# Kernel tuning notes

Hardware: AMD Instinct MI355X
Metric: run time of the kernel (lower is better)

The kernel has to match this reference:

```python
import math
import jax, jax.numpy as jnp
import numpy as np

B, S, D, H, DK, DV = 4, 2048, 512, 8, 64, 64

def setup_inputs() -> dict:
    key = jax.random.key(0)
    ks = jax.random.split(key, 6)
    x = jax.random.normal(ks[0], (B, S, D), jnp.float32)
    W_Q = jax.random.normal(ks[1], (H, D, DK), jnp.float32) / D
    W_K = jax.random.normal(ks[2], (H, D, DK), jnp.float32) / D
    W_V = jax.random.normal(ks[3], (H, D, DV), jnp.float32) / D
    W_G = jax.random.normal(ks[4], (D, H * DV), jnp.float32) / D
    W_O = jax.random.normal(ks[5], (H * DV, D), jnp.float32) / D
    return {"x": x, "W_Q": W_Q, "W_K": W_K, "W_V": W_V, "W_G": W_G, "W_O": W_O}

def _decay_matrix(n_heads, seq_len, dtype):
    # gammas per head, exactly as in __init__
    gammas = 1.0 - jnp.exp(jnp.linspace(math.log(1.0 / 32), math.log(1.0 / 512), n_heads))
    n = jnp.arange(seq_len)
    diff = n[:, None] - n[None, :]                      # [S,S]
    mask = diff >= 0
    safe = jnp.where(mask, diff, 0)
    dec = jnp.where(mask[None], gammas[:, None, None].astype(dtype) ** safe[None], 0.0)
    return dec                                           # [H,S,S]

def reference(x, W_Q, W_K, W_V, W_G, W_O):
    Bx, Sx, Dx = x.shape
    Hn = W_Q.shape[0]
    dv = W_V.shape[-1]
    # per-head projections (all heads vectorized)
    Q = jnp.einsum('bsd,hdk->bhsk', x, W_Q)
    K = jnp.einsum('bsd,hdk->bhsk', x, W_K)
    V = jnp.einsum('bsd,hdv->bhsv', x, W_V)
    Dmat = _decay_matrix(Hn, Sx, x.dtype)                # [H,S,S] causal decay
    # retention scores: QK^T elementwise-weighted by decay (no softmax)
    A = jnp.einsum('bhsk,bhtk->bhst', Q, K) * Dmat[None]  # [B,H,S,S] == self_retentions
    ret = jnp.einsum('bhst,bhtv->bhsv', A, V)            # [B,H,S,dv]
    out_heads = ret.transpose(0, 2, 1, 3).reshape(Bx, Sx, Hn * dv)  # concat over heads
    # GroupNorm(num_groups=H, num_channels=H) applied to reshape(-1, H):
    # each group has exactly 1 element -> mean == x, var == 0 -> output is 0.
    eps = 1e-5
    flat = out_heads.reshape(-1, Hn)
    mean = flat
    var = jnp.zeros_like(flat)
    Y = ((flat - mean) * jax.lax.rsqrt(var + eps)).reshape(out_heads.shape)
    # swish-gated output projection
    g = x @ W_G
    out = (g * jax.nn.sigmoid(g) * Y) @ W_O              # [B,S,D]
    return out, A
```

## Files before the change

kernel.cpp:

```cpp
#include <hip/hip_runtime.h>
#include <hip/hip_bf16.h>
#include <math.h>

#define B_ 4
#define S_ 2048
#define D_ 512
#define H_ 8
#define DK_ 64

typedef __bf16 bf16x8 __attribute__((ext_vector_type(8)));
typedef float f32x16 __attribute__((ext_vector_type(16)));
typedef float f32x4 __attribute__((ext_vector_type(4)));

static __device__ __forceinline__ unsigned short f2bf(float f) {
    unsigned int u = __builtin_bit_cast(unsigned int, f);
    unsigned int r = (u + 0x7FFFu + ((u >> 16) & 1u)) >> 16;
    return (unsigned short)r;
}

__global__ __launch_bounds__(256) void k_setup(const float* __restrict__ wq, const float* __restrict__ wk,
                                               unsigned short* __restrict__ wqT, unsigned short* __restrict__ wkT,
                                               float* __restrict__ tab, float* __restrict__ out0) {
    const int bx = blockIdx.x;
    if (bx < 2048) {
        int idx = bx * 256 + threadIdx.x;
        const int n = H_ * DK_ * D_;
        const float* src = idx < n ? wq : wk;
        unsigned short* dst = idx < n ? wqT : wkT;
        int o = idx < n ? idx : idx - n;
        int d  = o % D_;
        int hk = o / D_;
        int k  = hk % DK_;
        int h  = hk / DK_;
        dst[o] = f2bf(src[(h * D_ + d) * DK_ + k]);
    } else if (bx < 2112) {
        int i = (bx - 2048) * 256 + threadIdx.x;
        if (i < H_ * S_) {
            int h = i / S_;
            int n = i % S_;
            double xv = -3.4657359027997265 - (double)h * (2.772588722239781 / 7.0);
            double g = 1.0 - exp(xv);
            tab[i] = (float)pow(g, (double)n);
        }
    } else {
        f32x4* base = reinterpret_cast<f32x4*>(out0) + (size_t)(bx - 2112) * 32768;
        f32x4 z = {0.f, 0.f, 0.f, 0.f};
#pragma unroll
        for (int j = 0; j < 128; ++j)
            base[threadIdx.x + j * 256] = z;
    }
}

__global__ __launch_bounds__(256) void k_fill_upper(float* __restrict__ aout) {
    const int bh = blockIdx.y;
    f32x4 z = {0.f, 0.f, 0.f, 0.f};
    int r = blockIdx.x;
    int g = 0, cum = 0;
    for (; g < 7; ++g) { int cnt = 4 * (7 - g); if (r < cum + cnt) break; cum += cnt; }
    const int rr  = r - cum;
    const int per = 7 - g;
    const int panel = g * 4 + rr / per;
    const int st    = g + 1 + rr % per;

    float* base = aout + (size_t)bh * S_ * S_ + (size_t)(panel * 64) * S_ + st * 256;
    const int t = threadIdx.x;
#pragma unroll
    for (int j = 0; j < 16; ++j) {
        int u = t + j * 256;
        int row = u >> 6;
        int c4  = u & 63;
        *reinterpret_cast<f32x4*>(base + (size_t)row * S_ + c4 * 4) = z;
    }
}

__global__ __launch_bounds__(256, 2) void k_proj(const float* __restrict__ x,
                                                 const unsigned short* __restrict__ wqT,
                                                 const unsigned short* __restrict__ wkT,
                                                 unsigned short* __restrict__ qb,
                                                 unsigned short* __restrict__ kb) {
    const int tid  = threadIdx.x;
    const int lane = tid & 63;
    const int wave = tid >> 6;
    const int m0   = blockIdx.x * 32;
    const int half = blockIdx.y;
    const unsigned short* wt = half ? wkT : wqT;
    unsigned short* outp     = half ? kb  : qb;

    __shared__ unsigned short atile[32 * 520];

    {
        const float4* xsrc = reinterpret_cast<const float4*>(x + (size_t)m0 * D_);
#pragma unroll
        for (int i = 0; i < 16; ++i) {
            int u   = tid + i * 256;
            int row = u >> 7, c4 = u & 127;
            float4 v = xsrc[u];
            ushort4 o;
            o.x = f2bf(v.x); o.y = f2bf(v.y); o.z = f2bf(v.z); o.w = f2bf(v.w);
            *reinterpret_cast<ushort4*>(&atile[row * 520 + c4 * 4]) = o;
        }
    }
    __syncthreads();

    const int row  = lane & 31;
    const int col  = lane & 31;
    const int hi   = lane >> 5;
    const int koff = hi * 8;
    const int n0   = wave * 128;

    const unsigned short* b0 = wt + (size_t)(n0 +  0 + row) * D_ + koff;
    const unsigned short* b1 = wt + (size_t)(n0 + 32 + row) * D_ + koff;
    const unsigned short* b2 = wt + (size_t)(n0 + 64 + row) * D_ + koff;
    const unsigned short* b3 = wt + (size_t)(n0 + 96 + row) * D_ + koff;
    const unsigned short* ap = atile + row * 520 + koff;

    f32x16 acc0 = {}, acc1 = {}, acc2 = {}, acc3 = {};
#pragma unroll
    for (int kk = 0; kk < D_; kk += 16) {
        bf16x8 a = *reinterpret_cast<const bf16x8*>(ap + kk);
        acc0 = __builtin_amdgcn_mfma_f32_32x32x16_bf16(a, *reinterpret_cast<const bf16x8*>(b0 + kk), acc0, 0, 0, 0);
        acc1 = __builtin_amdgcn_mfma_f32_32x32x16_bf16(a, *reinterpret_cast<const bf16x8*>(b1 + kk), acc1, 0, 0, 0);
        acc2 = __builtin_amdgcn_mfma_f32_32x32x16_bf16(a, *reinterpret_cast<const bf16x8*>(b2 + kk), acc2, 0, 0, 0);
        acc3 = __builtin_amdgcn_mfma_f32_32x32x16_bf16(a, *reinterpret_cast<const bf16x8*>(b3 + kk), acc3, 0, 0, 0);
    }

#define EPI(ACC, NB) { \
    int n = n0 + (NB) * 32 + col; \
    int hh = n >> 6, k = n & 63; \
    _Pragma("unroll") \
    for (int r = 0; r < 16; ++r) { \
        int rowD = (r & 3) + 8 * (r >> 2) + 4 * hi; \
        int m = m0 + rowD; \
        int bidx = m >> 11, s = m & 2047; \
        outp[(((size_t)bidx * H_ + hh) * S_ + s) * DK_ + k] = f2bf(ACC[r]); \
    } }
    EPI(acc0, 0) EPI(acc1, 1) EPI(acc2, 2) EPI(acc3, 3)
#undef EPI
}

__global__ __launch_bounds__(256) void k_score(const unsigned short* __restrict__ qb,
                                               const unsigned short* __restrict__ kb,
                                               const float* __restrict__ tab,
                                               float* __restrict__ aout) {
    const int lane = threadIdx.x & 63;
    const int w    = threadIdx.x >> 6;
    const int id   = blockIdx.x;
    const int c    = id & 7, sidx = id >> 3;
    const int bh   = (c >> 1) + 4 * (sidx >> 3);
    const int p    = ((sidx & 7) << 1) | (c & 1);
    const int h    = bh & (H_ - 1);
    float* ablk = aout + (size_t)bh * S_ * S_;
    const float* th = tab + h * S_;

    __shared__ float tile[64 * 256];

    const int col  = lane & 31;
    const int hi   = lane >> 5;
    const int koff = hi * 8;

    const float c1 = 1.0f / th[col];
    float grc[16];
    int rowDv[16];
#pragma unroll
    for (int r = 0; r < 16; ++r) {
        rowDv[r] = (r & 3) + 8 * (r >> 2) + 4 * hi;
        grc[r] = th[rowDv[r]] * c1;
    }

    for (int pp = 0; pp < 2; ++pp) {
        const int panel = pp ? (31 - p) : p;
        const int s0 = panel * 64;
        const int qq = panel >> 2;
        const int rb = panel & 3;

        bf16x8 qf[2][4];
#pragma unroll
        for (int rg = 0; rg < 2; ++rg) {
            const unsigned short* qp = qb + ((size_t)bh * S_ + s0 + rg * 32 + col) * DK_ + koff;
#pragma unroll
            for (int i = 0; i < 4; ++i)
                qf[rg][i] = *reinterpret_cast<const bf16x8*>(qp + 16 * i);
        }

        for (int st = 0; st <= qq; ++st) {
            const int t0 = st * 256;
            const int ct0 = t0 + w * 64;
            const bool active = (st < qq) || (w <= rb);
            if (active) {
                f32x16 acc[2][2] = {{{}, {}}, {{}, {}}};
#pragma unroll
                for (int cg = 0; cg < 2; ++cg) {
                    const unsigned short* kp = kb + ((size_t)bh * S_ + ct0 + cg * 32 + col) * DK_ + koff;
                    bf16x8 kf0 = *reinterpret_cast<const bf16x8*>(kp);
                    bf16x8 kf1 = *reinterpret_cast<const bf16x8*>(kp + 16);
                    bf16x8 kf2 = *reinterpret_cast<const bf16x8*>(kp + 32);
                    bf16x8 kf3 = *reinterpret_cast<const bf16x8*>(kp + 48);
#pragma unroll
                    for (int rg = 0; rg < 2; ++rg) {
                        acc[rg][cg] = __builtin_amdgcn_mfma_f32_32x32x16_bf16(qf[rg][0], kf0, acc[rg][cg], 0, 0, 0);
                        acc[rg][cg] = __builtin_amdgcn_mfma_f32_32x32x16_bf16(qf[rg][1], kf1, acc[rg][cg], 0, 0, 0);
                        acc[rg][cg] = __builtin_amdgcn_mfma_f32_32x32x16_bf16(qf[rg][2], kf2, acc[rg][cg], 0, 0, 0);
                        acc[rg][cg] = __builtin_amdgcn_mfma_f32_32x32x16_bf16(qf[rg][3], kf3, acc[rg][cg], 0, 0, 0);
                    }
                }
                if (st < qq || w < rb) {
#pragma unroll
                    for (int rg = 0; rg < 2; ++rg) {
#pragma unroll
                        for (int cg = 0; cg < 2; ++cg) {
                            const float sc = th[s0 + rg * 32 - ct0 - cg * 32];
#pragma unroll
                            for (int r = 0; r < 16; ++r)
                                tile[(rg * 32 + rowDv[r]) * 256 + w * 64 + cg * 32 + col] =
                                    acc[rg][cg][r] * grc[r] * sc;
                        }
                    }
                } else {
#pragma unroll
                    for (int rg = 0; rg < 2; ++rg) {
#pragma unroll
                        for (int cg = 0; cg < 2; ++cg) {
                            const int dbase = 32 * (rg - cg);
#pragma unroll
                            for (int r = 0; r < 16; ++r) {
                                int d = dbase + rowDv[r] - col;
                                float v = (d >= 0) ? acc[rg][cg][r] * th[d] : 0.0f;
                                tile[(rg * 32 + rowDv[r]) * 256 + w * 64 + cg * 32 + col] = v;
                            }
                        }
                    }
                }
            } else {
                f32x4 z = {0.f, 0.f, 0.f, 0.f};
#pragma unroll
                for (int i = 0; i < 16; ++i) {
                    int r = i * 4 + (lane >> 4);
                    int cc = (lane & 15) * 4;
                    *reinterpret_cast<f32x4*>(&tile[r * 256 + w * 64 + cc]) = z;
                }
            }
            __syncthreads();
#pragma unroll
            for (int r = 0; r < 16; ++r) {
                int row = w * 16 + r;
                f32x4 v = *reinterpret_cast<const f32x4*>(&tile[row * 256 + lane * 4]);
                *reinterpret_cast<f32x4*>(ablk + (size_t)(s0 + row) * S_ + t0 + lane * 4) = v;
            }
            __syncthreads();
        }
    }
}

extern "C" void kernel_launch(void* const* d_in, const int* in_sizes, int n_in,
                              void* d_out, int out_size, void* d_ws, size_t ws_size,
                              hipStream_t stream) {
    const float* x  = (const float*)d_in[0];
    const float* wq = (const float*)d_in[1];
    const float* wk = (const float*)d_in[2];

    char* ws = (char*)d_ws;
    unsigned short* wqT = (unsigned short*)(ws);
    unsigned short* wkT = (unsigned short*)(ws + 524288);
    unsigned short* qb  = (unsigned short*)(ws + 1048576);
    unsigned short* kb  = (unsigned short*)(ws + 9437184);
    float*          tab = (float*)(ws + 17825792);

    float* out0 = (float*)d_out;
    float* aout = (float*)d_out + (size_t)B_ * S_ * D_;

    hipLaunchKernelGGL(k_setup, dim3(2144), dim3(256), 0, stream,
                       wq, wk, wqT, wkT, tab, out0);
    hipLaunchKernelGGL(k_proj, dim3(B_*S_/32, 2), dim3(256), 0, stream,
                       x, wqT, wkT, qb, kb);
    hipLaunchKernelGGL(k_score, dim3(512), dim3(256), 0, stream,
                       qb, kb, tab, aout);
    hipLaunchKernelGGL(k_fill_upper, dim3(112, 32), dim3(256), 0, stream, aout);
}
```

Baseline: 178.3 us.

## Fuse upper-triangle zero fill and output zeroing into score kernel

Merges the separate upper-triangle zero-fill kernel and the out0 zeroing into the score kernel. Each of the 512 blocks zero-fills 7 upper tiles plus a slice of out0, with odd blocks filling before scoring and even blocks after, so zero stores overlap with compute in other blocks. This removes one kernel launch and the tail between kernels, but makes each score block do more store work.

After: 166.8 us. 1.07x faster.

```diff
diff --git a/kernel.cpp b/kernel.cpp
--- a/kernel.cpp
+++ b/kernel.cpp
@@ -20,7 +20,7 @@
 
 __global__ __launch_bounds__(256) void k_setup(const float* __restrict__ wq, const float* __restrict__ wk,
                                                unsigned short* __restrict__ wqT, unsigned short* __restrict__ wkT,
-                                               float* __restrict__ tab, float* __restrict__ out0) {
+                                               float* __restrict__ tab) {
     const int bx = blockIdx.x;
     if (bx < 2048) {
         int idx = bx * 256 + threadIdx.x;
@@ -33,7 +33,7 @@
         int k  = hk % DK_;
         int h  = hk / DK_;
         dst[o] = f2bf(src[(h * D_ + d) * DK_ + k]);
-    } else if (bx < 2112) {
+    } else {
         int i = (bx - 2048) * 256 + threadIdx.x;
         if (i < H_ * S_) {
             int h = i / S_;
@@ -42,34 +42,6 @@
             double g = 1.0 - exp(xv);
             tab[i] = (float)pow(g, (double)n);
         }
-    } else {
-        f32x4* base = reinterpret_cast<f32x4*>(out0) + (size_t)(bx - 2112) * 32768;
-        f32x4 z = {0.f, 0.f, 0.f, 0.f};
-#pragma unroll
-        for (int j = 0; j < 128; ++j)
-            base[threadIdx.x + j * 256] = z;
-    }
-}
-
-__global__ __launch_bounds__(256) void k_fill_upper(float* __restrict__ aout) {
-    const int bh = blockIdx.y;
-    f32x4 z = {0.f, 0.f, 0.f, 0.f};
-    int r = blockIdx.x;
-    int g = 0, cum = 0;
-    for (; g < 7; ++g) { int cnt = 4 * (7 - g); if (r < cum + cnt) break; cum += cnt; }
-    const int rr  = r - cum;
-    const int per = 7 - g;
-    const int panel = g * 4 + rr / per;
-    const int st    = g + 1 + rr % per;
-
-    float* base = aout + (size_t)bh * S_ * S_ + (size_t)(panel * 64) * S_ + st * 256;
-    const int t = threadIdx.x;
-#pragma unroll
-    for (int j = 0; j < 16; ++j) {
-        int u = t + j * 256;
-        int row = u >> 6;
-        int c4  = u & 63;
-        *reinterpret_cast<f32x4*>(base + (size_t)row * S_ + c4 * 4) = z;
     }
 }
 
@@ -138,21 +110,17 @@
 #undef EPI
 }
 
-__global__ __launch_bounds__(256) void k_score(const unsigned short* __restrict__ qb,
-                                               const unsigned short* __restrict__ kb,
-                                               const float* __restrict__ tab,
-                                               float* __restrict__ aout) {
-    const int lane = threadIdx.x & 63;
-    const int w    = threadIdx.x >> 6;
-    const int id   = blockIdx.x;
+static __device__ __forceinline__ void score_part(int id, int tid,
+        const unsigned short* __restrict__ qb, const unsigned short* __restrict__ kb,
+        const float* __restrict__ tab, float* __restrict__ aout, float* tile) {
+    const int lane = tid & 63;
+    const int w    = tid >> 6;
     const int c    = id & 7, sidx = id >> 3;
     const int bh   = (c >> 1) + 4 * (sidx >> 3);
     const int p    = ((sidx & 7) << 1) | (c & 1);
     const int h    = bh & (H_ - 1);
     float* ablk = aout + (size_t)bh * S_ * S_;
     const float* th = tab + h * S_;
-
-    __shared__ float tile[64 * 256];
 
     const int col  = lane & 31;
     const int hi   = lane >> 5;
@@ -251,6 +219,52 @@
     }
 }
 
+static __device__ __forceinline__ void fill_part(int bid, int tid,
+        float* __restrict__ aout, float* __restrict__ out0) {
+    f32x4 z = {0.f, 0.f, 0.f, 0.f};
+#pragma unroll 1
+    for (int i = 0; i < 7; ++i) {
+        const int f = bid * 7 + i;
+        const int bh = f / 112;
+        int r = f % 112;
+        int g = 0, cum = 0;
+        for (; g < 7; ++g) { int cnt = 4 * (7 - g); if (r < cum + cnt) break; cum += cnt; }
+        const int rr  = r - cum;
+        const int per = 7 - g;
+        const int panel = g * 4 + rr / per;
+        const int st    = g + 1 + rr % per;
+        float* base = aout + (size_t)bh * S_ * S_ + (size_t)(panel * 64) * S_ + st * 256;
+#pragma unroll
+        for (int j = 0; j < 16; ++j) {
+            int u = tid + j * 256;
+            int row = u >> 6;
+            int c4  = u & 63;
+            *reinterpret_cast<f32x4*>(base + (size_t)row * S_ + c4 * 4) = z;
+        }
+    }
+    f32x4* b0 = reinterpret_cast<f32x4*>(out0) + (size_t)bid * 2048;
+#pragma unroll
+    for (int j = 0; j < 8; ++j)
+        b0[tid + j * 256] = z;
+}
+
+__global__ __launch_bounds__(256) void k_scorefill(const unsigned short* __restrict__ qb,
+                                                   const unsigned short* __restrict__ kb,
+                                                   const float* __restrict__ tab,
+                                                   float* __restrict__ aout,
+                                                   float* __restrict__ out0) {
+    __shared__ __align__(16) float tile[64 * 256];
+    const int bid = blockIdx.x;
+    const int tid = threadIdx.x;
+    if (bid & 1) {
+        fill_part(bid, tid, aout, out0);
+        score_part(bid, tid, qb, kb, tab, aout, tile);
+    } else {
+        score_part(bid, tid, qb, kb, tab, aout, tile);
+        fill_part(bid, tid, aout, out0);
+    }
+}
+
 extern "C" void kernel_launch(void* const* d_in, const int* in_sizes, int n_in,
                               void* d_out, int out_size, void* d_ws, size_t ws_size,
                               hipStream_t stream) {
@@ -268,11 +282,10 @@
     float* out0 = (float*)d_out;
     float* aout = (float*)d_out + (size_t)B_ * S_ * D_;
 
-    hipLaunchKernelGGL(k_setup, dim3(2144), dim3(256), 0, stream,
-                       wq, wk, wqT, wkT, tab, out0);
+    hipLaunchKernelGGL(k_setup, dim3(2112), dim3(256), 0, stream,
+                       wq, wk, wqT, wkT, tab);
     hipLaunchKernelGGL(k_proj, dim3(B_*S_/32, 2), dim3(256), 0, stream,
                        x, wqT, wkT, qb, kb);
-    hipLaunchKernelGGL(k_score, dim3(512), dim3(256), 0, stream,
-                       qb, kb, tab, aout);
-    hipLaunchKernelGGL(k_fill_upper, dim3(112, 32), dim3(256), 0, stream, aout);
-}
+    hipLaunchKernelGGL(k_scorefill, dim3(512), dim3(256), 0, stream,
+                       qb, kb, tab, aout, out0);
+}
```
